# Kernel tuning notes

Hardware: AMD Instinct MI355X
Metric: run time of the kernel (lower is better)

Reference implementation:

```python
import jax, jax.numpy as jnp
import numpy as np

B, T, F = 256, 192, 8
CARD0, CARD1 = 1000, 100
E0, E1 = 32, 16
H = 512
D_IN = F + E0 + E1  # 56


def _glorot(key, shape):
    fan_in, fan_out = shape[0], shape[-1]
    lim = jnp.sqrt(6.0 / (fan_in + fan_out))
    return jax.random.uniform(key, shape, jnp.float32, -lim, lim)


def setup_inputs() -> dict:
    key = jax.random.key(0)
    ks = jax.random.split(key, 16)
    return {
        "x_cont": jax.random.normal(ks[0], (B, T, F), jnp.float32),
        "cat0": jax.random.randint(ks[1], (B, T), 0, CARD0),
        "cat1": jax.random.randint(ks[2], (B, T), 0, CARD1),
        "emb0": _glorot(ks[3], (CARD0, E0)),
        "emb1": _glorot(ks[4], (CARD1, E1)),
        "Wk1": _glorot(ks[5], (D_IN, 4 * H)),
        "Wr1": _glorot(ks[6], (H, 4 * H)),
        "b1": jnp.zeros((4 * H,), jnp.float32).at[H:2 * H].set(1.0),  # unit_forget_bias
        "Wk2": _glorot(ks[7], (H, 4 * H)),
        "Wr2": _glorot(ks[8], (H, 4 * H)),
        "b2": jnp.zeros((4 * H,), jnp.float32).at[H:2 * H].set(1.0),
        "Wmu": _glorot(ks[9], (H, 1)),
        "bmu": _glorot(ks[10], (1, 1))[0],
        "Wsig": _glorot(ks[11], (H, 1)),
        "bsig": _glorot(ks[12], (1, 1))[0],
    }


def _lstm(x, Wk, Wr, b):
    # x: [B, T, D]; Keras gate order i, f, g(c), o; zero initial states (inference mode,
    # dropout/recurrent_dropout inactive when training=False).
    xz = jnp.einsum('btd,dk->btk', x, Wk) + b  # precompute input projection for all steps
    h0 = jnp.zeros((x.shape[0], H), x.dtype)

    def step(carry, z_t):
        h, c = carry
        z = z_t + h @ Wr  # [B, 4H]
        i, f, g, o = jnp.split(z, 4, axis=-1)
        i = jax.nn.sigmoid(i)
        f = jax.nn.sigmoid(f)
        g = jnp.tanh(g)
        o = jax.nn.sigmoid(o)
        c = f * c + i * g
        h = o * jnp.tanh(c)
        return (h, c), h

    _, hs = jax.lax.scan(step, (h0, h0), jnp.swapaxes(xz, 0, 1))  # [T, B, H]
    return jnp.swapaxes(hs, 0, 1)


def reference(x_cont, cat0, cat1, emb0, emb1, Wk1, Wr1, b1, Wk2, Wr2, b2, Wmu, bmu, Wsig, bsig):
    x = jnp.concatenate([x_cont, emb0[cat0], emb1[cat1]], axis=-1)  # [B, T, 56]
    x = _lstm(x, Wk1, Wr1, b1)
    x = _lstm(x, Wk2, Wr2, b2)
    mu = x @ Wmu + bmu                      # count_data=False -> raw mu
    sigma = jax.nn.softplus(x @ Wsig + bsig)
    return (mu, sigma)
```

## Files before the change

### kernel.cpp

```cpp
#include <hip/hip_runtime.h>
#include <math.h>

#define Bsz 256
#define Tsz 192
#define Fc 8
#define E0c 32
#define E1c 16
#define Hc 512
#define G4 2048
#define DINP 64
#define K1t 576
#define K2t 1024
#define NBLK 256
#define KPAD1 584
#define KPAD2 1032
#define LDSB_BYTES (64 * KPAD2 * 2)
#define SLOT_STRIDE 16
#define RING_U (64 * SLOT_STRIDE)
#define WD_WAIT (1 << 17)

typedef __attribute__((ext_vector_type(8))) short short8;
typedef __attribute__((ext_vector_type(4))) float f32x4;

template<int N> struct IC { static constexpr int v = N; };
template<int C, int CMAX, typename F>
__device__ __forceinline__ void static_for(F&& f) {
    if constexpr (C < CMAX) {
        f(IC<C>{});
        static_for<C + 1, CMAX>(f);
    }
}

static __device__ __forceinline__ float bf2f(ushort u) {
    return __uint_as_float(((uint)u) << 16);
}
static __device__ __forceinline__ ushort f2bf(float f) {
    uint u = __float_as_uint(f);
    u = (u + 0x7fffu + ((u >> 16) & 1u)) >> 16;
    return (ushort)u;
}

static __device__ __forceinline__ uint poll_sc1(const uint* p) {
    uint v;
    asm volatile("global_load_dword %0, %1, off sc1\n\t"
                 "s_waitcnt vmcnt(0)"
                 : "=v"(v) : "v"((unsigned long long)p) : "memory");
    return v;
}
static __device__ __forceinline__ void store_slot_sc1(uint* p, uint v) {
    asm volatile("global_store_dword %0, %1, off sc1"
                 :: "v"((unsigned long long)p), "v"(v) : "memory");
}

__global__ __launch_bounds__(256) void build_x_kernel(
    const float* __restrict__ x_cont, const int* __restrict__ cat0,
    const int* __restrict__ cat1, const float* __restrict__ emb0,
    const float* __restrict__ emb1, ushort* __restrict__ x_bf)
{
    int idx = blockIdx.x * 256 + threadIdx.x;
    if (idx >= Tsz * Bsz * DINP) return;
    int d = idx & 63;
    int row = idx >> 6;
    int t = row >> 8;
    int b = row & 255;
    float v = 0.f;
    if (d < Fc)                  v = x_cont[(b * Tsz + t) * Fc + d];
    else if (d < Fc + E0c)       v = emb0[cat0[b * Tsz + t] * E0c + (d - Fc)];
    else if (d < Fc + E0c + E1c) v = emb1[cat1[b * Tsz + t] * E1c + (d - Fc - E0c)];
    x_bf[idx] = f2bf(v);
}

__global__ __launch_bounds__(256) void transpose_w_kernel(
    const float* __restrict__ in, ushort* __restrict__ out, int K, int ldout, int coff)
{
    __shared__ float tile[32][33];
    int k0 = blockIdx.x * 32;
    int n0 = blockIdx.y * 32;
    int tx = threadIdx.x & 31, ty = threadIdx.x >> 5;
    #pragma unroll
    for (int p = 0; p < 4; ++p) {
        int k = k0 + ty + p * 8;
        tile[ty + p * 8][tx] = (k < K) ? in[k * G4 + n0 + tx] : 0.f;
    }
    __syncthreads();
    #pragma unroll
    for (int p = 0; p < 4; ++p) {
        int nl = ty + p * 8;
        out[(size_t)(n0 + nl) * ldout + coff + k0 + tx] = f2bf(tile[tx][nl]);
    }
}

static __device__ __forceinline__ void wait_slots(const uint* arr, uint tg) {
    const uint* p = arr + (threadIdx.x & 31) * SLOT_STRIDE;
    int it = 0;
    while (true) {
        uint v = poll_sc1(p);
        if (__all((int)(v >= tg))) break;
        if (++it >= WD_WAIT) break;
        __builtin_amdgcn_s_sleep(1);
    }
}

template<int KS_IN, int KS_TOT, int LDA_IN, int KPADv, bool HAS_DEP, int FANOUT>
static __device__ __forceinline__ void run_layer(
    const ushort* __restrict__ Ain,
    ushort* __restrict__ hbuf,
    const ushort* __restrict__ hz,
    const ushort* __restrict__ Wt,
    const float* __restrict__ bias,
    ushort* B_lds,
    uint* pflags,
    int g, int jb, int m0, int j0)
{
    constexpr int KS_R = KS_TOT - KS_IN;
    constexpr int KL = KS_TOT * 32;
    constexpr int SEGS = KL / 8;
    int tid = threadIdx.x;
    int lane = tid & 63, wv = tid >> 6;
    int lane15 = lane & 15, quad = lane >> 4;
    int bid = jb * 8 + g * 2 + (HAS_DEP ? 1 : 0);

    uint* ring = pflags + (size_t)(bid * 4 + wv) * RING_U;
    const uint* own_arr = ring;
    const uint* dep_arr = ring + 32 * SLOT_STRIDE;

    uint* pub_dst;
    {
        int j = lane & 31;
        int cons_role = HAS_DEP ? 1 : (lane >> 5);
        int cons_bid = j * 8 + g * 2 + cons_role;
        pub_dst = pflags + (size_t)(cons_bid * 4 + wv) * RING_U
                + ((lane >= 32) ? 32 * SLOT_STRIDE : 0) + jb * SLOT_STRIDE;
    }

    for (int i = tid; i < 64 * SEGS; i += 256) {
        int row = i / SEGS, seg = i - row * SEGS;
        int gz = (row >> 4) * Hc + j0 + (row & 15);
        *(uint4*)&B_lds[row * KPADv + seg * 8] =
            *(const uint4*)(Wt + (size_t)gz * KL + seg * 8);
    }
    __syncthreads();

    float bgate[4];
    #pragma unroll
    for (int gt = 0; gt < 4; ++gt) bgate[gt] = bias[gt * Hc + j0 + lane15];
    float cst[4] = {0.f, 0.f, 0.f, 0.f};

    int arow = m0 + wv * 16 + lane15;
    int crow0 = m0 + wv * 16 + quad * 4;

    for (int t = 0; t < Tsz; ++t) {
        f32x4 acc[4];
        #pragma unroll
        for (int gt = 0; gt < 4; ++gt) acc[gt] = (f32x4){0.f, 0.f, 0.f, 0.f};

        if constexpr (HAS_DEP) {
            wait_slots(dep_arr, (uint)(t + 1));
        }
        {
            const ushort* p0 = Ain + ((size_t)t * Bsz + arow) * LDA_IN + quad * 8;
            uint4 bufA[KS_IN];
            static_for<0, KS_IN>([&](auto Kc) {
                constexpr int ks = decltype(Kc)::v;
                bufA[ks] = *(const uint4*)(p0 + ks * 32);
            });
            asm volatile("" ::: "memory");
            static_for<0, KS_IN>([&](auto Kc) {
                constexpr int ks = decltype(Kc)::v;
                short8 av = __builtin_bit_cast(short8, bufA[ks]);
                #pragma unroll
                for (int gt = 0; gt < 4; ++gt) {
                    short8 bfr = *(const short8*)&B_lds[(gt * 16 + lane15) * KPADv + ks * 32 + quad * 8];
                    acc[gt] = __builtin_amdgcn_mfma_f32_16x16x32_bf16(av, bfr, acc[gt], 0, 0, 0);
                }
            });
        }

        if (t) wait_slots(own_arr, (uint)t);
        {
            const ushort* p1base = (t > 0) ? (hbuf + (size_t)(t - 1) * Bsz * Hc) : hz;
            const ushort* p1 = p1base + (size_t)arow * Hc + quad * 8;
            uint4 bufB[KS_R];
            static_for<0, KS_R>([&](auto Kc) {
                constexpr int ks = decltype(Kc)::v;
                bufB[ks] = *(const uint4*)(p1 + ks * 32);
            });
            asm volatile("" ::: "memory");
            static_for<0, KS_R>([&](auto Kc) {
                constexpr int ks = decltype(Kc)::v;
                short8 av = __builtin_bit_cast(short8, bufB[ks]);
                #pragma unroll
                for (int gt = 0; gt < 4; ++gt) {
                    short8 bfr = *(const short8*)&B_lds[(gt * 16 + lane15) * KPADv + (KS_IN + ks) * 32 + quad * 8];
                    acc[gt] = __builtin_amdgcn_mfma_f32_16x16x32_bf16(av, bfr, acc[gt], 0, 0, 0);
                }
            });
        }

        uint hv[4];
        #pragma unroll
        for (int r = 0; r < 4; ++r) {
            float zi = acc[0][r] + bgate[0];
            float zf = acc[1][r] + bgate[1];
            float zg = acc[2][r] + bgate[2];
            float zo = acc[3][r] + bgate[3];
            float ig = 1.f / (1.f + __expf(-zi));
            float fg = 1.f / (1.f + __expf(-zf));
            float gg = tanhf(zg);
            float og = 1.f / (1.f + __expf(-zo));
            float cn = fg * cst[r] + ig * gg;
            cst[r] = cn;
            float hn = og * tanhf(cn);
            hv[r] = (uint)f2bf(hn);
        }
        {
            unsigned long long hb = (unsigned long long)
                &hbuf[((size_t)t * Bsz + crow0) * Hc + j0 + lane15];
            asm volatile(
                "global_store_short %0, %1, off sc1\n\t"
                "global_store_short %0, %2, off offset:1024 sc1\n\t"
                "global_store_short %0, %3, off offset:2048 sc1\n\t"
                "global_store_short %0, %4, off offset:3072 sc1\n\t"
                "s_waitcnt vmcnt(0)"
                :: "v"(hb), "v"(hv[0]), "v"(hv[1]), "v"(hv[2]), "v"(hv[3])
                : "memory");
        }
        if (lane < FANOUT)
            store_slot_sc1(pub_dst, (uint)(t + 1));
    }
}

__global__ __launch_bounds__(256, 1) void deepar_persistent(
    const ushort* __restrict__ x_bf,
    const ushort* __restrict__ Wt1, const ushort* __restrict__ Wt2,
    const float* __restrict__ b1, const float* __restrict__ b2,
    ushort* __restrict__ h1, ushort* __restrict__ h2,
    const ushort* __restrict__ hz,
    const float* __restrict__ Wmu, const float* __restrict__ bmu,
    const float* __restrict__ Wsig, const float* __restrict__ bsig,
    float* __restrict__ out, uint* __restrict__ pflags)
{
    extern __shared__ ushort B_lds[];

    int bid = blockIdx.x;
    int xcd = bid & 7;
    int g = xcd >> 1;
    int role = xcd & 1;
    int jb = bid >> 3;
    int m0 = g * 64;
    int j0 = jb * 16;

    if (role == 0) {
        run_layer<2, 18, DINP, KPAD1, false, 64>(x_bf, h1, hz, Wt1, b1, B_lds,
                                                 pflags, g, jb, m0, j0);
        return;
    }
    run_layer<16, 32, Hc, KPAD2, true, 32>(h1, h2, hz, Wt2, b2, B_lds,
                                           pflags, g, jb, m0, j0);

    {
        int wv = threadIdx.x >> 6;
        const uint* ring = pflags + (size_t)(bid * 4 + wv) * RING_U;
        wait_slots(ring, (uint)Tsz);
    }
    __syncthreads();

    int lane = threadIdx.x & 63, wv = threadIdx.x >> 6;
    float wm[8], wsg[8];
    #pragma unroll
    for (int i = 0; i < 8; ++i) {
        wm[i] = Wmu[lane * 8 + i];
        wsg[i] = Wsig[lane * 8 + i];
    }
    float bmu0 = bmu[0], bsg0 = bsig[0];
    for (int i = jb * 4 + wv; i < 64 * Tsz; i += 128) {
        int b = m0 + (i & 63);
        int t = i >> 6;
        const ushort* hp = h2 + ((size_t)t * Bsz + b) * Hc + lane * 8;
        short8 hvv = *(const short8*)hp;
        float smu = 0.f, ssg = 0.f;
        #pragma unroll
        for (int e = 0; e < 8; ++e) {
            float f = bf2f((ushort)hvv[e]);
            smu += f * wm[e];
            ssg += f * wsg[e];
        }
        #pragma unroll
        for (int off = 32; off > 0; off >>= 1) {
            smu += __shfl_down(smu, off, 64);
            ssg += __shfl_down(ssg, off, 64);
        }
        if (lane == 0) {
            int oi = b * Tsz + t;
            float sg = ssg + bsg0;
            float sp = sg > 0.f ? sg + log1pf(__expf(-sg)) : log1pf(__expf(sg));
            out[oi] = smu + bmu0;
            out[Bsz * Tsz + oi] = sp;
        }
    }
}

extern "C" void kernel_launch(void* const* d_in, const int* in_sizes, int n_in,
                              void* d_out, int out_size, void* d_ws, size_t ws_size,
                              hipStream_t stream) {
    const float* x_cont = (const float*)d_in[0];
    const int*   cat0   = (const int*)d_in[1];
    const int*   cat1   = (const int*)d_in[2];
    const float* emb0   = (const float*)d_in[3];
    const float* emb1   = (const float*)d_in[4];
    const float* Wk1    = (const float*)d_in[5];
    const float* Wr1    = (const float*)d_in[6];
    const float* b1     = (const float*)d_in[7];
    const float* Wk2    = (const float*)d_in[8];
    const float* Wr2    = (const float*)d_in[9];
    const float* b2     = (const float*)d_in[10];
    const float* Wmu    = (const float*)d_in[11];
    const float* bmu    = (const float*)d_in[12];
    const float* Wsig   = (const float*)d_in[13];
    const float* bsig   = (const float*)d_in[14];
    float* out = (float*)d_out;

    const size_t pflags_bytes = (size_t)NBLK * 4 * RING_U * 4;

    char* ws = (char*)d_ws;
    uint*   pflags = (uint*)ws;                                ws += pflags_bytes;
    ushort* x_bf  = (ushort*)ws;                               ws += (size_t)Tsz * Bsz * DINP * 2;
    ushort* Wt1   = (ushort*)ws;                               ws += (size_t)G4 * K1t * 2;
    ushort* Wt2   = (ushort*)ws;                               ws += (size_t)G4 * K2t * 2;
    ushort* h1    = (ushort*)ws;                               ws += (size_t)Tsz * Bsz * Hc * 2;
    ushort* h2    = (ushort*)ws;                               ws += (size_t)Tsz * Bsz * Hc * 2;
    ushort* hz    = (ushort*)ws;                               ws += (size_t)Bsz * Hc * 2;

    hipMemsetAsync(pflags, 0, pflags_bytes, stream);
    hipMemsetAsync(hz, 0, (size_t)Bsz * Hc * 2, stream);

    build_x_kernel<<<(Tsz * Bsz * DINP + 255) / 256, 256, 0, stream>>>(
        x_cont, cat0, cat1, emb0, emb1, x_bf);
    transpose_w_kernel<<<dim3(2, 64), 256, 0, stream>>>(Wk1, Wt1, 56, K1t, 0);
    transpose_w_kernel<<<dim3(16, 64), 256, 0, stream>>>(Wr1, Wt1, Hc, K1t, DINP);
    transpose_w_kernel<<<dim3(16, 64), 256, 0, stream>>>(Wk2, Wt2, Hc, K2t, 0);
    transpose_w_kernel<<<dim3(16, 64), 256, 0, stream>>>(Wr2, Wt2, Hc, K2t, Hc);

    hipFuncSetAttribute((const void*)deepar_persistent,
                        hipFuncAttributeMaxDynamicSharedMemorySize, LDSB_BYTES);
    deepar_persistent<<<dim3(NBLK), dim3(256), LDSB_BYTES, stream>>>(
        x_bf, Wt1, Wt2, b1, b2, h1, h2, hz, Wmu, bmu, Wsig, bsig, out, pflags);
}
```

Measured before the change: 1.195 ms.

## Split recurrent wait into half-ready phases and use fast rcp activations

Flag waits now ballot which producer slots are ready. When not all 32 are ready, the kernel waits for the first 16 producers, runs the MFMAs over that half of K, then waits for the rest. The point is to overlap compute with waiting on slower producers inside the per-timestep dependency chain. Sigmoid and tanh also switch to exp plus hardware rcp instead of division and tanhf. This shortens the serial per-step tail but adds a small approximation error and may add branch overhead.

Result: no change. 1.195 ms, median of 2 (+0.0%).

```diff
diff --git a/kernel.cpp b/kernel.cpp
--- a/kernel.cpp
+++ b/kernel.cpp
@@ -40,6 +40,13 @@
     return (ushort)u;
 }
 
+static __device__ __forceinline__ float sigm_f(float x) {
+    return __builtin_amdgcn_rcpf(1.f + __expf(-x));
+}
+static __device__ __forceinline__ float tanh_f(float x) {
+    return 1.f - 2.f * __builtin_amdgcn_rcpf(1.f + __expf(2.f * x));
+}
+
 static __device__ __forceinline__ uint poll_sc1(const uint* p) {
     uint v;
     asm volatile("global_load_dword %0, %1, off sc1\n\t"
@@ -90,14 +97,57 @@
     }
 }
 
-static __device__ __forceinline__ void wait_slots(const uint* arr, uint tg) {
-    const uint* p = arr + (threadIdx.x & 31) * SLOT_STRIDE;
+static __device__ __forceinline__ uint poll_mask(const uint* arr, uint tg) {
+    uint v = poll_sc1(arr + (threadIdx.x & 31) * SLOT_STRIDE);
+    unsigned long long bal = __ballot((int)(v >= tg));
+    return (uint)bal;
+}
+static __device__ __forceinline__ void wait_mask(const uint* arr, uint tg, uint need) {
     int it = 0;
-    while (true) {
-        uint v = poll_sc1(p);
-        if (__all((int)(v >= tg))) break;
+    while ((poll_mask(arr, tg) & need) != need) {
         if (++it >= WD_WAIT) break;
         __builtin_amdgcn_s_sleep(1);
+    }
+}
+static __device__ __forceinline__ void wait_all(const uint* arr, uint tg) {
+    wait_mask(arr, tg, 0xFFFFFFFFu);
+}
+
+template<int C0, int C1, int KOFF, int KPADv>
+static __device__ __forceinline__ void load_mfma_range(
+    const ushort* p, const ushort* B_lds, int lane15, int quad, f32x4* acc)
+{
+    uint4 buf[C1 - C0];
+    static_for<C0, C1>([&](auto Kc) {
+        constexpr int ks = decltype(Kc)::v;
+        buf[ks - C0] = *(const uint4*)(p + ks * 32);
+    });
+    asm volatile("" ::: "memory");
+    static_for<C0, C1>([&](auto Kc) {
+        constexpr int ks = decltype(Kc)::v;
+        short8 av = __builtin_bit_cast(short8, buf[ks - C0]);
+        #pragma unroll
+        for (int gt = 0; gt < 4; ++gt) {
+            short8 bfr = *(const short8*)&B_lds[(gt * 16 + lane15) * KPADv
+                                               + (KOFF + ks) * 32 + quad * 8];
+            acc[gt] = __builtin_amdgcn_mfma_f32_16x16x32_bf16(av, bfr, acc[gt], 0, 0, 0);
+        }
+    });
+}
+
+template<int KOFF, int KPADv>
+static __device__ __forceinline__ void gated_phase16(
+    const ushort* p, const uint* arr, uint tg,
+    const ushort* B_lds, int lane15, int quad, f32x4* acc)
+{
+    uint m = poll_mask(arr, tg);
+    if (m == 0xFFFFFFFFu) {
+        load_mfma_range<0, 16, KOFF, KPADv>(p, B_lds, lane15, quad, acc);
+    } else {
+        wait_mask(arr, tg, 0x0000FFFFu);
+        load_mfma_range<0, 8, KOFF, KPADv>(p, B_lds, lane15, quad, acc);
+        wait_mask(arr, tg, 0xFFFF0000u);
+        load_mfma_range<8, 16, KOFF, KPADv>(p, B_lds, lane15, quad, acc);
     }
 }
 
@@ -154,47 +204,25 @@
         #pragma unroll
         for (int gt = 0; gt < 4; ++gt) acc[gt] = (f32x4){0.f, 0.f, 0.f, 0.f};
 
-        if constexpr (HAS_DEP) {
-            wait_slots(dep_arr, (uint)(t + 1));
-        }
         {
             const ushort* p0 = Ain + ((size_t)t * Bsz + arow) * LDA_IN + quad * 8;
-            uint4 bufA[KS_IN];
-            static_for<0, KS_IN>([&](auto Kc) {
-                constexpr int ks = decltype(Kc)::v;
-                bufA[ks] = *(const uint4*)(p0 + ks * 32);
-            });
-            asm volatile("" ::: "memory");
-            static_for<0, KS_IN>([&](auto Kc) {
-                constexpr int ks = decltype(Kc)::v;
-                short8 av = __builtin_bit_cast(short8, bufA[ks]);
-                #pragma unroll
-                for (int gt = 0; gt < 4; ++gt) {
-                    short8 bfr = *(const short8*)&B_lds[(gt * 16 + lane15) * KPADv + ks * 32 + quad * 8];
-                    acc[gt] = __builtin_amdgcn_mfma_f32_16x16x32_bf16(av, bfr, acc[gt], 0, 0, 0);
-                }
-            });
-        }
-
-        if (t) wait_slots(own_arr, (uint)t);
+            if constexpr (HAS_DEP) {
+                gated_phase16<0, KPADv>(p0, dep_arr, (uint)(t + 1),
+                                        B_lds, lane15, quad, acc);
+            } else {
+                load_mfma_range<0, KS_IN, 0, KPADv>(p0, B_lds, lane15, quad, acc);
+            }
+        }
+
         {
-            const ushort* p1base = (t > 0) ? (hbuf + (size_t)(t - 1) * Bsz * Hc) : hz;
-            const ushort* p1 = p1base + (size_t)arow * Hc + quad * 8;
-            uint4 bufB[KS_R];
-            static_for<0, KS_R>([&](auto Kc) {
-                constexpr int ks = decltype(Kc)::v;
-                bufB[ks] = *(const uint4*)(p1 + ks * 32);
-            });
-            asm volatile("" ::: "memory");
-            static_for<0, KS_R>([&](auto Kc) {
-                constexpr int ks = decltype(Kc)::v;
-                short8 av = __builtin_bit_cast(short8, bufB[ks]);
-                #pragma unroll
-                for (int gt = 0; gt < 4; ++gt) {
-                    short8 bfr = *(const short8*)&B_lds[(gt * 16 + lane15) * KPADv + (KS_IN + ks) * 32 + quad * 8];
-                    acc[gt] = __builtin_amdgcn_mfma_f32_16x16x32_bf16(av, bfr, acc[gt], 0, 0, 0);
-                }
-            });
+            if (t == 0) {
+                const ushort* p1 = hz + (size_t)arow * Hc + quad * 8;
+                load_mfma_range<0, KS_R, KS_IN, KPADv>(p1, B_lds, lane15, quad, acc);
+            } else {
+                const ushort* p1 = hbuf + ((size_t)(t - 1) * Bsz + arow) * Hc + quad * 8;
+                gated_phase16<KS_IN, KPADv>(p1, own_arr, (uint)t,
+                                            B_lds, lane15, quad, acc);
+            }
         }
 
         uint hv[4];
@@ -204,13 +232,13 @@
             float zf = acc[1][r] + bgate[1];
             float zg = acc[2][r] + bgate[2];
             float zo = acc[3][r] + bgate[3];
-            float ig = 1.f / (1.f + __expf(-zi));
-            float fg = 1.f / (1.f + __expf(-zf));
-            float gg = tanhf(zg);
-            float og = 1.f / (1.f + __expf(-zo));
+            float ig = sigm_f(zi);
+            float fg = sigm_f(zf);
+            float gg = tanh_f(zg);
+            float og = sigm_f(zo);
             float cn = fg * cst[r] + ig * gg;
             cst[r] = cn;
-            float hn = og * tanhf(cn);
+            float hn = og * tanh_f(cn);
             hv[r] = (uint)f2bf(hn);
         }
         {
@@ -261,7 +289,7 @@
     {
         int wv = threadIdx.x >> 6;
         const uint* ring = pflags + (size_t)(bid * 4 + wv) * RING_U;
-        wait_slots(ring, (uint)Tsz);
+        wait_all(ring, (uint)Tsz);
     }
     __syncthreads();
 
```
